# Performance work log

Measured on AMD Instinct MI355X. Metric: run time of the kernel, lower is better.

Reference implementation:

```python
import math
import jax, jax.numpy as jnp
import numpy as np

B, NP = 256, 3
LAT, TXT, D = 512, 768, 768
NL = 6
DI, DS, DC = 2 * D, 16, 4
DTR = math.ceil(D / 16)
EPS = 1e-5


def _silu(x):
    return x * jax.nn.sigmoid(x)


def _layernorm(x, g, b):
    m = x.mean(-1, keepdims=True)
    v = ((x - m) ** 2).mean(-1, keepdims=True)
    return (x - m) / jnp.sqrt(v + EPS) * g + b


def _mamba(x, in_w, conv_w, conv_b, xproj_w, dt_w, dt_b, Alog, Dp, out_w):
    # x: [B, L, D]; standard Mamba(d_state=16, d_conv=4, expand=2)
    Bb, L, _ = x.shape
    xz = jnp.einsum('bld,ed->ble', x, in_w)          # [B, L, 2*DI]
    u, z = jnp.split(xz, 2, axis=-1)
    # depthwise causal conv (kernel DC, left pad DC-1, truncated to L)
    up = jnp.pad(u, ((0, 0), (DC - 1, 0), (0, 0)))
    uc = conv_b + sum(conv_w[:, k] * up[:, k:k + L, :] for k in range(DC))
    uc = _silu(uc)
    xdbl = jnp.einsum('bld,ed->ble', uc, xproj_w)    # [B, L, DTR+2*DS]
    dt, Bm, Cm = jnp.split(xdbl, [DTR, DTR + DS], axis=-1)
    dt = jax.nn.softplus(jnp.einsum('blr,dr->bld', dt, dt_w) + dt_b)  # [B,L,DI]
    A = -jnp.exp(Alog)                               # [DI, DS]

    def step(h, xs):
        dt_t, B_t, C_t, u_t = xs                     # [B,DI],[B,DS],[B,DS],[B,DI]
        dA = jnp.exp(dt_t[..., None] * A)            # [B,DI,DS]
        h = h * dA + (dt_t * u_t)[..., None] * B_t[:, None, :]
        y = jnp.einsum('bds,bs->bd', h, C_t)
        return h, y

    h0 = jnp.zeros((Bb, DI, DS), x.dtype)
    xs = (dt.transpose(1, 0, 2), Bm.transpose(1, 0, 2),
          Cm.transpose(1, 0, 2), uc.transpose(1, 0, 2))
    _, ys = jax.lax.scan(step, h0, xs)
    y = ys.transpose(1, 0, 2) + Dp * uc
    y = y * _silu(z)
    return jnp.einsum('bld,ed->ble', y, out_w)       # [B, L, D]


def _forward(z_noisy, timestep, text_emb,
             zin_w, zin_b, tin_w, tin_b, time_w, time_b, part_emb,
             local_w, local_b, f_w, f_b, fuse_w, fuse_b, final_w, final_b,
             ln_g, ln_b, m_in_w, m_conv_w, m_conv_b, m_xproj_w, m_dt_w,
             m_dt_b, m_Alog, m_Dp, m_out_w, oln_g, oln_b, zout_w, zout_b):
    z_feat = jnp.einsum('bpl,dl->bpd', z_noisy, zin_w) + zin_b + part_emb
    text_feat = (text_emb @ tin_w.T + tin_b)[:, None]            # [B,1,D]
    half = D // 2
    freqs = jnp.exp(-math.log(10000.0) * jnp.arange(half, dtype=jnp.float32) / half)
    targ = timestep.astype(jnp.float32)[:, None] * freqs
    temb = jnp.concatenate([jnp.cos(targ), jnp.sin(targ)], -1)   # [B,D]
    time_feat = (temb @ time_w.T + time_b)[:, None]              # [B,1,D]
    x = jnp.concatenate([time_feat, text_feat, z_feat], 1)       # [B,5,D]
    # sinusoidal position embedding (first 5 rows of max_len=10 table)
    pos = jnp.arange(5, dtype=jnp.float32)[:, None]
    div = jnp.exp(jnp.arange(0, D, 2, dtype=jnp.float32) * (-math.log(10000.0) / D))
    pe = jnp.zeros((5, D), jnp.float32)
    pe = pe.at[:, 0::2].set(jnp.sin(pos * div)).at[:, 1::2].set(jnp.cos(pos * div))
    x = x + pe[None]
    text_cond = x[:, 1, :]                                       # [B,D]
    for i in range(NL):
        residual = x
        xl = _silu(jnp.einsum('bld,ed->ble', x, local_w[i]) + local_b[i])
        y_rep = jnp.broadcast_to(text_cond[:, None, :], xl.shape)
        yhat = jnp.einsum('bld,ed->ble', jnp.concatenate([xl, y_rep], -1), f_w[i]) + f_b[i]
        y_gate = y_rep * jax.nn.sigmoid(yhat)
        xt = jnp.einsum('bld,ed->ble', jnp.concatenate([xl, y_gate], -1), fuse_w[i]) + fuse_b[i]
        mf = lambda v, d: _mamba(v, m_in_w[i, d], m_conv_w[i, d], m_conv_b[i, d],
                                 m_xproj_w[i, d], m_dt_w[i, d], m_dt_b[i, d],
                                 m_Alog[i, d], m_Dp[i, d], m_out_w[i, d])
        xf = mf(xt, 0)
        xb = jnp.flip(mf(jnp.flip(xt, 1), 1), 1)
        xo = jnp.einsum('bld,ed->ble', jnp.concatenate([xf, xb], -1), final_w[i]) + final_b[i]
        x = _layernorm(xo + residual, ln_g[i], ln_b[i])
    z_out = x[:, 2:, :]                                          # [B,3,D]
    return jnp.einsum('bpd,ld->bpl', _layernorm(z_out, oln_g, oln_b), zout_w) + zout_b


def setup_inputs() -> dict:
    key = jax.random.key(0)
    kit = iter(jax.random.split(key, 40))

    def rn(shape, s=0.02):
        return jax.random.normal(next(kit), shape, jnp.float32) * s

    inp = dict(
        z_noisy=jax.random.normal(next(kit), (B, NP, LAT), jnp.float32),
        text_emb=jax.random.normal(next(kit), (B, TXT), jnp.float32),
        zin_w=rn((D, LAT)), zin_b=jnp.zeros((D,), jnp.float32),
        tin_w=rn((D, TXT)), tin_b=jnp.zeros((D,), jnp.float32),
        time_w=rn((D, D)), time_b=jnp.zeros((D,), jnp.float32),
        part_emb=rn((1, NP, D)),
        local_w=rn((NL, D, D)), local_b=jnp.zeros((NL, D), jnp.float32),
        f_w=rn((NL, D, 2 * D)), f_b=jnp.zeros((NL, D), jnp.float32),
        fuse_w=rn((NL, D, 2 * D)), fuse_b=jnp.zeros((NL, D), jnp.float32),
        final_w=rn((NL, D, 2 * D)), final_b=jnp.zeros((NL, D), jnp.float32),
        ln_g=jnp.ones((NL, D), jnp.float32), ln_b=jnp.zeros((NL, D), jnp.float32),
        m_in_w=rn((NL, 2, 2 * DI, D)),
        m_conv_w=rn((NL, 2, DI, DC), 0.1),
        m_conv_b=jnp.zeros((NL, 2, DI), jnp.float32),
        m_xproj_w=rn((NL, 2, DTR + 2 * DS, DI)),
        m_dt_w=rn((NL, 2, DI, DTR), 0.1),
        m_dt_b=jnp.full((NL, 2, DI), -4.6, jnp.float32),
        m_Alog=jnp.tile(jnp.log(jnp.arange(1, DS + 1, dtype=jnp.float32)), (NL, 2, DI, 1)),
        m_Dp=jnp.ones((NL, 2, DI), jnp.float32),
        m_out_w=rn((NL, 2, D, DI)),
        oln_g=jnp.ones((D,), jnp.float32), oln_b=jnp.zeros((D,), jnp.float32),
        zout_w=rn((LAT, D)), zout_b=jnp.zeros((LAT,), jnp.float32),
        timestep=jax.random.randint(next(kit), (B,), 0, 1000),
    )
    return inp


def reference(z_noisy, text_emb, zin_w, zin_b, tin_w, tin_b, time_w, time_b,
              part_emb, local_w, local_b, f_w, f_b, fuse_w, fuse_b, final_w,
              final_b, ln_g, ln_b, m_in_w, m_conv_w, m_conv_b, m_xproj_w,
              m_dt_w, m_dt_b, m_Alog, m_Dp, m_out_w, oln_g, oln_b, zout_w,
              zout_b, timestep):
    return _forward(z_noisy, timestep, text_emb, zin_w, zin_b, tin_w, tin_b,
                    time_w, time_b, part_emb, local_w, local_b, f_w, f_b,
                    fuse_w, fuse_b, final_w, final_b, ln_g, ln_b, m_in_w,
                    m_conv_w, m_conv_b, m_xproj_w, m_dt_w, m_dt_b, m_Alog,
                    m_Dp, m_out_w, oln_g, oln_b, zout_w, zout_b)
```

## Files before the change

### kernel.cpp

```cpp
#include <hip/hip_runtime.h>
#include <hip/hip_bf16.h>
#include <math.h>

#define B_   256
#define NP_  3
#define LAT_ 512
#define TXT_ 768
#define D_   768
#define NL_  6
#define DI_  1536
#define DS_  16
#define DC_  4
#define DTR_ 48
#define L_   5
#define M_   (B_*L_)
#define EPS_ 1e-5f

#define OB_WBF    0ull
#define OB_XPP    139591680ull
#define OB_TEMB   144310272ull
#define OB_ZNORM  144703488ull
#define OB_XBF    145883136ull
#define OB_TCBF   147849216ull
#define OB_CAT1   148242432ull
#define OB_XTBF   152174592ull
#define OB_XZBF   154140672ull
#define OB_UCY    169869312ull
#define OB_CAT2   177733632ull
#define OB_X      181665792ull
#define OB_TC     185597952ull
#define OB_ZFEAT  187170816ull
#define OB_XO     189530112ull
#define OB_PART   193462272ull

#define WO_LOCAL  0u
#define WO_F      3538944u
#define WO_FUSE   10616832u
#define WO_FINAL  17694720u
#define WO_IN     24772608u
#define WO_OUT    53084160u
#define WO_ZIN    67239936u
#define WO_TIN    67633152u
#define WO_TIME   68222976u
#define WO_ZOUT   68812800u
#define WO_ZNOISY 69206016u
#define WO_TEXT   69599232u
#define WO_END    69795840u

#define CVT_BLOCKS  17040u
#define XPAD_BLOCKS 1152u
#define TEMB_BLOCKS 384u
#define PREP_BLOCKS (CVT_BLOCKS + XPAD_BLOCKS + TEMB_BLOCKS)

typedef __attribute__((ext_vector_type(4))) float floatx4;
typedef __attribute__((ext_vector_type(8))) short short8;
typedef __attribute__((ext_vector_type(8))) unsigned short ushort8v;
typedef __attribute__((ext_vector_type(4))) unsigned short ushort4v;

__device__ __forceinline__ float sigm(float v) { return 1.f / (1.f + expf(-v)); }
__device__ __forceinline__ float softplus(float v) {
    return fmaxf(v, 0.f) + log1pf(expf(-fabsf(v)));
}
__device__ __forceinline__ unsigned short bf16rn(float f) {
    unsigned int u = __builtin_bit_cast(unsigned int, f);
    u = (u + 0x7fffu + ((u >> 16) & 1u)) >> 16;
    return (unsigned short)u;
}
__device__ __forceinline__ float b2f(unsigned short u) {
    unsigned int x = ((unsigned int)u) << 16;
    return __builtin_bit_cast(float, x);
}

template<int N> __device__ __forceinline__ void waitv() {
    asm volatile("s_waitcnt vmcnt(%0)" :: "i"(N) : "memory");
}

struct CvtArgs { const float* s[12]; };

__global__ __launch_bounds__(256) void prep_kernel(
    CvtArgs a, unsigned short* __restrict__ dst,
    const float* __restrict__ xw, unsigned short* __restrict__ xpd,
    const int* __restrict__ ts, unsigned short* __restrict__ temb)
{
    unsigned bid = blockIdx.x;
    if (bid < CVT_BLOCKS) {
        constexpr unsigned ends[12] = {
            3538944u, 10616832u, 17694720u, 24772608u, 53084160u, 67239936u,
            67633152u, 68222976u, 68812800u, 69206016u, 69599232u, 69795840u };
        const unsigned wv = (bid * 256u + threadIdx.x) >> 6;
        const unsigned lane = threadIdx.x & 63u;
        const unsigned wbase = wv * 1024u;
        unsigned idxq[4];
        floatx4 v[4];
#pragma unroll
        for (int q = 0; q < 4; ++q) {
            unsigned gbase = wbase + (unsigned)q * 256u;
            int t = 0;
            while (gbase >= ends[t]) ++t;
            unsigned start = t ? ends[t - 1] : 0u;
            idxq[q] = gbase + lane * 4u;
            v[q] = __builtin_nontemporal_load((const floatx4*)(a.s[t] + (idxq[q] - start)));
        }
#pragma unroll
        for (int q = 0; q < 4; ++q) {
            ushort4v o = { bf16rn(v[q][0]), bf16rn(v[q][1]), bf16rn(v[q][2]), bf16rn(v[q][3]) };
            __builtin_nontemporal_store(o, (ushort4v*)(dst + idxq[q]));
        }
    } else if (bid < CVT_BLOCKS + XPAD_BLOCKS) {
        unsigned i8 = ((bid - CVT_BLOCKS) * 256u + threadIdx.x) * 8u;
        if (i8 >= 12u * 128u * 1536u) return;
        unsigned pi = i8 / (128u * 1536u);
        unsigned rem = i8 - pi * 128u * 1536u;
        unsigned row = rem / 1536u, col = rem - row * 1536u;
        ushort8v o = {0, 0, 0, 0, 0, 0, 0, 0};
        if (row < 80u) {
            const float* s = xw + ((size_t)pi * 80u + row) * 1536u + col;
            floatx4 v0 = __builtin_nontemporal_load((const floatx4*)s);
            floatx4 v1 = __builtin_nontemporal_load((const floatx4*)(s + 4));
            o = ushort8v{ bf16rn(v0[0]), bf16rn(v0[1]), bf16rn(v0[2]), bf16rn(v0[3]),
                          bf16rn(v1[0]), bf16rn(v1[1]), bf16rn(v1[2]), bf16rn(v1[3]) };
        }
        *(ushort8v*)(xpd + i8) = o;
    } else {
        int idx = (bid - CVT_BLOCKS - XPAD_BLOCKS) * 256 + threadIdx.x;
        if (idx >= B_ * 384) return;
        int j = idx % 384, b = idx / 384;
        float f = expf(-logf(10000.f) * (float)j / 384.f);
        float targ = (float)ts[b] * f;
        temb[(size_t)b * D_ + j]       = bf16rn(cosf(targ));
        temb[(size_t)b * D_ + 384 + j] = bf16rn(sinf(targ));
    }
}

template<int BM, int BN, int CD, int DEPTH, int PF>
__global__ __launch_bounds__(256) void gemm_bf16_kernel(
    const unsigned short* __restrict__ A, int lda,
    const unsigned short* __restrict__ W, int wld,
    const float* __restrict__ bias,
    const float* __restrict__ aux0,
    const float* __restrict__ aux1,
    void* __restrict__ Cv, int ldc,
    int M, int N, int K, int epi, int ncap,
    int zsplit, unsigned long long zA, unsigned long long zW, unsigned long long zC)
{
    constexpr int GA = BM / 64;
    constexpr int GB = BN / 64;
    constexpr int LPS = GA + GB;
    constexpr int FRM = BM / 32;
    constexpr int FRN = BN / 32;
    constexpr int BMSK = DEPTH - 1;

    const int z = blockIdx.z;
    const int dirz = z / zsplit, ksz = z - dirz * zsplit;
    A += (unsigned long long)dirz * zA + (unsigned long long)ksz * (unsigned)K;
    W += (unsigned long long)dirz * zW + (unsigned long long)ksz * (unsigned)K;

    __shared__ unsigned short lds[DEPTH][(BM + BN) * 32];

    const int tid = threadIdx.x;
    const int m0 = blockIdx.y * BM, n0 = blockIdx.x * BN;
    const int w = tid >> 6, lane = tid & 63;
    const int wr = w >> 1, wc = w & 1;
    const int lrow = lane & 15;
    const int lk = (lane >> 4) << 3;

    const int rA = tid >> 2, sA = tid & 3;
    const int scA = ((sA ^ ((rA >> 1) & 3)) << 3);
    floatx4 acc[FRM][FRN] = {};

    auto stage = [&](int buf, int k0) {
        unsigned short* base = &lds[buf][0];
#pragma unroll
        for (int i = 0; i < GA; ++i) {
            int t = tid + i * 256;
            int r = t >> 2;
            const unsigned short* src = A + (size_t)(m0 + r) * lda + k0 + scA;
            __builtin_amdgcn_global_load_lds(
                (const __attribute__((address_space(1))) unsigned int*)(const void*)src,
                (__attribute__((address_space(3))) unsigned int*)(void*)(base + i * 2048 + w * 512),
                16, 0, 0);
        }
#pragma unroll
        for (int i = 0; i < GB; ++i) {
            int t = tid + i * 256;
            int r = t >> 2;
            const unsigned short* src = W + (size_t)(n0 + r) * wld + k0 + scA;
            __builtin_amdgcn_global_load_lds(
                (const __attribute__((address_space(1))) unsigned int*)(const void*)src,
                (__attribute__((address_space(3))) unsigned int*)(void*)(base + BM * 32 + i * 2048 + w * 512),
                16, 0, 0);
        }
    };

    const int nt = K >> 5;
#pragma unroll
    for (int s = 0; s < PF; ++s)
        if (s < nt) stage(s, s << 5);

    int offA[FRM], offB[FRN];
#pragma unroll
    for (int i = 0; i < FRM; ++i) {
        int row = wr * (BM / 2) + i * 16 + lrow;
        offA[i] = row * 32 + (lk ^ (((row >> 1) & 3) << 3));
    }
#pragma unroll
    for (int j = 0; j < FRN; ++j) {
        int row = wc * (BN / 2) + j * 16 + lrow;
        offB[j] = BM * 32 + row * 32 + (lk ^ (((row >> 1) & 3) << 3));
    }

    for (int t = 0; t < nt; ++t) {
        int rem = nt - 1 - t;
        if (rem >= PF) { stage((t + PF) & BMSK, (t + PF) << 5); waitv<PF * LPS>(); }
        else if (rem == 5) waitv<5 * LPS>();
        else if (rem == 4) waitv<4 * LPS>();
        else if (rem == 3) waitv<3 * LPS>();
        else if (rem == 2) waitv<2 * LPS>();
        else if (rem == 1) waitv<1 * LPS>();
        else               waitv<0>();
        __builtin_amdgcn_s_barrier();
        const unsigned short* pl = &lds[t & BMSK][0];
        short8 af[FRM], bfv[FRN];
#pragma unroll
        for (int i = 0; i < FRM; ++i) af[i] = *(const short8*)(pl + offA[i]);
#pragma unroll
        for (int j = 0; j < FRN; ++j) bfv[j] = *(const short8*)(pl + offB[j]);
#pragma unroll
        for (int i = 0; i < FRM; ++i)
#pragma unroll
            for (int j = 0; j < FRN; ++j)
                acc[i][j] = __builtin_amdgcn_mfma_f32_16x16x32_bf16(af[i], bfv[j], acc[i][j], 0, 0, 0);
    }

#pragma unroll
    for (int i = 0; i < FRM; ++i) {
        int row0 = m0 + wr * (BM / 2) + i * 16 + (lane >> 4) * 4;
#pragma unroll
        for (int j = 0; j < FRN; ++j) {
            int col = n0 + wc * (BN / 2) + j * 16 + lrow;
            if (col >= ncap) continue;
            float bb = bias ? bias[col] : 0.f;
#pragma unroll
            for (int r = 0; r < 4; ++r) {
                int row = row0 + r;
                float v = acc[i][j][r] + bb;
                if (epi == 1) {
                    v = v * sigm(v);
                } else if (epi == 3) {
                    int b = row / 5;
                    v = acc[i][j][r] + bb + b2f(((const unsigned short*)aux0)[(size_t)b * 768 + col]);
                    v = aux1[(size_t)b * 768 + col] * sigm(v);
                }
                size_t off = (size_t)z * zC + (size_t)row * ldc + col;
                if (CD == 1) ((float*)Cv)[off] = v;
                else         ((unsigned short*)Cv)[off] = bf16rn(v);
            }
        }
    }
}

template<int CD, int DEPTH, int PF>
__global__ __launch_bounds__(512) void gemm512_kernel(
    const unsigned short* __restrict__ A, int lda,
    const unsigned short* __restrict__ W, int wld,
    const float* __restrict__ bias,
    const float* __restrict__ aux0,
    const float* __restrict__ aux1,
    void* __restrict__ Cv, int ldc,
    int M, int N, int K, int epi, int ncap,
    int zsplit, unsigned long long zA, unsigned long long zW, unsigned long long zC)
{
    constexpr int BMSK = DEPTH - 1;
    const int z = blockIdx.z;
    const int dirz = z / zsplit, ksz = z - dirz * zsplit;
    A += (unsigned long long)dirz * zA + (unsigned long long)ksz * (unsigned)K;
    W += (unsigned long long)dirz * zW + (unsigned long long)ksz * (unsigned)K;

    __shared__ unsigned short lds[DEPTH][128 * 32];

    const int tid = threadIdx.x;
    const int m0 = blockIdx.y * 64, n0 = blockIdx.x * 64;
    const int w = tid >> 6, lane = tid & 63;
    const int wr = w >> 1, wc = w & 1;
    const int lrow = lane & 15;
    const int lk = (lane >> 4) << 3;

    const int st = tid & 255;
    const int rA = st >> 2, sA = st & 3;
    const int scA = ((sA ^ ((rA >> 1) & 3)) << 3);
    const bool isA = (tid < 256);
    floatx4 acc[2] = {};

    auto stage = [&](int buf, int k0) {
        unsigned short* dstp = &lds[buf][0] + (isA ? w * 512 : 2048 + (w - 4) * 512);
        const unsigned short* src = isA
            ? A + (size_t)(m0 + rA) * lda + k0 + scA
            : W + (size_t)(n0 + rA) * wld + k0 + scA;
        __builtin_amdgcn_global_load_lds(
            (const __attribute__((address_space(1))) unsigned int*)(const void*)src,
            (__attribute__((address_space(3))) unsigned int*)(void*)dstp,
            16, 0, 0);
    };

    const int nt = K >> 5;
#pragma unroll
    for (int s = 0; s < PF; ++s)
        if (s < nt) stage(s, s << 5);

    const int rowA = wr * 16 + lrow;
    const int offA = rowA * 32 + (lk ^ (((rowA >> 1) & 3) << 3));
    int offB[2];
#pragma unroll
    for (int j = 0; j < 2; ++j) {
        int rowB = wc * 32 + j * 16 + lrow;
        offB[j] = 2048 + rowB * 32 + (lk ^ (((rowB >> 1) & 3) << 3));
    }

    for (int t = 0; t < nt; ++t) {
        int rem = nt - 1 - t;
        if (rem >= PF) { stage((t + PF) & BMSK, (t + PF) << 5); waitv<PF>(); }
        else if (rem == 5) waitv<5>();
        else if (rem == 4) waitv<4>();
        else if (rem == 3) waitv<3>();
        else if (rem == 2) waitv<2>();
        else if (rem == 1) waitv<1>();
        else               waitv<0>();
        __builtin_amdgcn_s_barrier();
        const unsigned short* pl = &lds[t & BMSK][0];
        short8 af = *(const short8*)(pl + offA);
        short8 b0 = *(const short8*)(pl + offB[0]);
        short8 b1 = *(const short8*)(pl + offB[1]);
        acc[0] = __builtin_amdgcn_mfma_f32_16x16x32_bf16(af, b0, acc[0], 0, 0, 0);
        acc[1] = __builtin_amdgcn_mfma_f32_16x16x32_bf16(af, b1, acc[1], 0, 0, 0);
    }

    int row0 = m0 + wr * 16 + (lane >> 4) * 4;
#pragma unroll
    for (int j = 0; j < 2; ++j) {
        int col = n0 + wc * 32 + j * 16 + lrow;
        if (col >= ncap) continue;
        float bb = bias ? bias[col] : 0.f;
#pragma unroll
        for (int r = 0; r < 4; ++r) {
            int row = row0 + r;
            float v = acc[j][r] + bb;
            if (epi == 1) {
                v = v * sigm(v);
            } else if (epi == 3) {
                int b = row / 5;
                v = acc[j][r] + bb + b2f(((const unsigned short*)aux0)[(size_t)b * 768 + col]);
                v = aux1[(size_t)b * 768 + col] * sigm(v);
            }
            size_t off = (size_t)z * zC + (size_t)row * ldc + col;
            if (CD == 1) ((float*)Cv)[off] = v;
            else         ((unsigned short*)Cv)[off] = bf16rn(v);
        }
    }
}

template<int DEPTH, int PF>
__global__ __launch_bounds__(512) void gemm512b_kernel(
    const unsigned short* __restrict__ A, int lda,
    const unsigned short* __restrict__ W, int wld,
    unsigned short* __restrict__ C, int ldc, int K)
{
    constexpr int BMSK = DEPTH - 1;
    __shared__ unsigned short lds[DEPTH][8192];

    const int tid = threadIdx.x;
    const int m0 = blockIdx.y * 128, n0 = blockIdx.x * 128;
    const int w = tid >> 6, lane = tid & 63;
    const int wr = w >> 2, wc = w & 3;
    const int lrow = lane & 15;
    const int lk = (lane >> 4) << 3;

    const int rA = tid >> 2, sA = tid & 3;
    const int scA = ((sA ^ ((rA >> 1) & 3)) << 3);
    floatx4 acc[4][2] = {};

    auto stage = [&](int buf, int k0) {
        unsigned short* base = &lds[buf][0];
        const unsigned short* srcA = A + (size_t)(m0 + rA) * lda + k0 + scA;
        __builtin_amdgcn_global_load_lds(
            (const __attribute__((address_space(1))) unsigned int*)(const void*)srcA,
            (__attribute__((address_space(3))) unsigned int*)(void*)(base + w * 512),
            16, 0, 0);
        const unsigned short* srcB = W + (size_t)(n0 + rA) * wld + k0 + scA;
        __builtin_amdgcn_global_load_lds(
            (const __attribute__((address_space(1))) unsigned int*)(const void*)srcB,
            (__attribute__((address_space(3))) unsigned int*)(void*)(base + 4096 + w * 512),
            16, 0, 0);
    };

    const int nt = K >> 5;
#pragma unroll
    for (int s = 0; s < PF; ++s)
        if (s < nt) stage(s, s << 5);

    int offA[4], offB[2];
#pragma unroll
    for (int i = 0; i < 4; ++i) {
        int row = wr * 64 + i * 16 + lrow;
        offA[i] = row * 32 + (lk ^ (((row >> 1) & 3) << 3));
    }
#pragma unroll
    for (int j = 0; j < 2; ++j) {
        int row = wc * 32 + j * 16 + lrow;
        offB[j] = 4096 + row * 32 + (lk ^ (((row >> 1) & 3) << 3));
    }

    for (int t = 0; t < nt; ++t) {
        int rem = nt - 1 - t;
        if (rem >= PF) { stage((t + PF) & BMSK, (t + PF) << 5); waitv<PF * 2>(); }
        else if (rem == 1) waitv<2>();
        else               waitv<0>();
        __builtin_amdgcn_s_barrier();
        const unsigned short* pl = &lds[t & BMSK][0];
        short8 af[4], bfv[2];
#pragma unroll
        for (int i = 0; i < 4; ++i) af[i] = *(const short8*)(pl + offA[i]);
#pragma unroll
        for (int j = 0; j < 2; ++j) bfv[j] = *(const short8*)(pl + offB[j]);
#pragma unroll
        for (int i = 0; i < 4; ++i)
#pragma unroll
            for (int j = 0; j < 2; ++j)
                acc[i][j] = __builtin_amdgcn_mfma_f32_16x16x32_bf16(af[i], bfv[j], acc[i][j], 0, 0, 0);
    }

#pragma unroll
    for (int i = 0; i < 4; ++i) {
        int row0 = m0 + wr * 64 + i * 16 + (lane >> 4) * 4;
#pragma unroll
        for (int j = 0; j < 2; ++j) {
            int col = n0 + wc * 32 + j * 16 + lrow;
#pragma unroll
            for (int r = 0; r < 4; ++r)
                C[(size_t)(row0 + r) * ldc + col] = bf16rn(acc[i][j][r]);
        }
    }
}

__global__ void finalize_embed_kernel(float* __restrict__ x,
                                      unsigned short* __restrict__ xbf,
                                      const float* __restrict__ zfeat,
                                      const float* __restrict__ part_emb,
                                      float* __restrict__ tc,
                                      unsigned short* __restrict__ tcbf)
{
    int idx = blockIdx.x * blockDim.x + threadIdx.x;
    if (idx >= B_ * L_ * D_) return;
    int d = idx % D_;
    int bl = idx / D_;
    int l = bl % L_, b = bl / L_;
    float v;
    if (l >= 2) v = zfeat[((size_t)(b * 3 + (l - 2))) * D_ + d] + part_emb[(size_t)(l - 2) * D_ + d];
    else        v = x[idx];
    int j = d >> 1;
    float dv = expf((float)(2 * j) * (-logf(10000.f) / (float)D_));
    float ang = (float)l * dv;
    v += (d & 1) ? cosf(ang) : sinf(ang);
    x[idx] = v;
    xbf[idx] = bf16rn(v);
    if (l == 1) { tc[(size_t)b * D_ + d] = v; tcbf[(size_t)b * D_ + d] = bf16rn(v); }
}

__global__ __launch_bounds__(256) void conv_silu_kernel(
    const unsigned short* __restrict__ xz,
    const float* __restrict__ cw,
    const float* __restrict__ cb,
    unsigned short* __restrict__ ucy)
{
    int idx = blockIdx.x * 256 + threadIdx.x;
    if (idx >= 2 * M_ * DI_ / 8) return;
    int c8 = (idx % (DI_ / 8)) * 8;
    int t2 = idx / (DI_ / 8);
    int bl = t2 % M_, dir = t2 / M_;
    int l = bl % L_, b = bl / L_;

    float acc[8];
    const float* cbp = cb + dir * DI_ + c8;
#pragma unroll
    for (int e = 0; e < 8; ++e) acc[e] = cbp[e];
    floatx4 w[8];
#pragma unroll
    for (int e = 0; e < 8; ++e)
        w[e] = *(const floatx4*)(cw + ((size_t)(dir * DI_ + c8 + e)) * DC_);
#pragma unroll
    for (int k = 0; k < DC_; ++k) {
        int lp = dir ? (l + 3 - k) : (l + k - 3);
        if (lp >= 0 && lp < L_) {
            ushort8v xv = *(const ushort8v*)(xz + ((size_t)(b * L_ + lp)) * 6144 + dir * 3072 + c8);
#pragma unroll
            for (int e = 0; e < 8; ++e) acc[e] = fmaf(w[e][k], b2f(xv[e]), acc[e]);
        }
    }
    ushort8v o;
#pragma unroll
    for (int e = 0; e < 8; ++e) { float v = acc[e]; o[e] = bf16rn(v * sigm(v)); }
    *(ushort8v*)(ucy + (size_t)idx * 8) = o;
}

__global__ __launch_bounds__(256) void dtscan_kernel(
    const float* __restrict__ part,
    unsigned short* ucy,
    const unsigned short* __restrict__ xz,
    const float* __restrict__ dt_w,
    const float* __restrict__ dt_b,
    const float* __restrict__ Alog,
    const float* __restrict__ Dp)
{
    __shared__ float xd[L_][80];
    const int dir = blockIdx.z;
    const int b = blockIdx.y;
    const int ch = blockIdx.x * 256 + threadIdx.x;

    for (int o = threadIdx.x; o < L_ * 80; o += 256) {
        int l = o / 80, n = o - l * 80;
        float s = 0.f;
#pragma unroll
        for (int ks = 0; ks < 8; ++ks)
            s += part[((size_t)(dir * 8 + ks) * M_ + b * L_ + l) * 80 + n];
        xd[l][n] = s;
    }
    __syncthreads();

    const int cg = dir * DI_ + ch;
    float dt[L_];
    const float* wp = dt_w + (size_t)cg * DTR_;
    float dbv = dt_b[cg];
#pragma unroll
    for (int l = 0; l < L_; ++l) {
        float v = dbv;
#pragma unroll
        for (int r = 0; r < DTR_; ++r) v = fmaf(xd[l][r], wp[r], v);
        dt[l] = softplus(v);
    }

    float Aa[DS_], h[DS_];
#pragma unroll
    for (int s = 0; s < DS_; ++s) { Aa[s] = -expf(Alog[(size_t)cg * DS_ + s]); h[s] = 0.f; }
    float Dv = Dp[cg];

#pragma unroll
    for (int t = 0; t < L_; ++t) {
        const int l = dir ? (L_ - 1 - t) : t;
        size_t base = (size_t)(b * L_ + l);
        size_t uoff = ((size_t)dir * M_ + base) * DI_ + ch;
        float dtv = dt[l];
        float ucv = b2f(ucy[uoff]);
        float du = dtv * ucv;
        float y = 0.f;
#pragma unroll
        for (int s = 0; s < DS_; ++s) {
            h[s] = h[s] * expf(dtv * Aa[s]) + du * xd[l][48 + s];
            y = fmaf(h[s], xd[l][64 + s], y);
        }
        float zv = b2f(xz[base * 6144 + dir * 3072 + 1536 + ch]);
        ucy[uoff] = bf16rn((y + Dv * ucv) * (zv * sigm(zv)));
    }
}

__device__ __forceinline__ float block_sum(float v)
{
    __shared__ float sd[4];
#pragma unroll
    for (int o = 1; o < 64; o <<= 1) v += __shfl_xor(v, o, 64);
    int lane = threadIdx.x & 63, wid = threadIdx.x >> 6;
    if (lane == 0) sd[wid] = v;
    __syncthreads();
    v = sd[0] + sd[1] + sd[2] + sd[3];
    __syncthreads();
    return v;
}

__global__ __launch_bounds__(256) void ln_residual_kernel(
    const float* __restrict__ xo, float* __restrict__ x,
    unsigned short* __restrict__ xbf,
    const float* __restrict__ g, const float* __restrict__ bt,
    const float* __restrict__ og, const float* __restrict__ ob,
    unsigned short* __restrict__ znorm, int do_out)
{
    int row = blockIdx.x;
    const float* pa = xo + (size_t)row * D_;
    float* px = x + (size_t)row * D_;
    float v[3];
    float s = 0.f;
#pragma unroll
    for (int i = 0; i < 3; ++i) { int d = threadIdx.x + 256 * i; v[i] = pa[d] + px[d]; s += v[i]; }
    float mean = block_sum(s) * (1.f / (float)D_);
    float sq = 0.f;
#pragma unroll
    for (int i = 0; i < 3; ++i) { float t = v[i] - mean; sq += t * t; }
    float var = block_sum(sq) * (1.f / (float)D_);
    float inv = rsqrtf(var + EPS_);
    float o[3];
#pragma unroll
    for (int i = 0; i < 3; ++i) {
        int d = threadIdx.x + 256 * i;
        o[i] = (v[i] - mean) * inv * g[d] + bt[d];
        px[d] = o[i];
        xbf[(size_t)row * D_ + d] = bf16rn(o[i]);
    }
    int l = row % L_;
    if (do_out && l >= 2) {
        int b = row / L_;
        float s2 = o[0] + o[1] + o[2];
        float mean2 = block_sum(s2) * (1.f / (float)D_);
        float sq2 = 0.f;
#pragma unroll
        for (int i = 0; i < 3; ++i) { float t = o[i] - mean2; sq2 += t * t; }
        float var2 = block_sum(sq2) * (1.f / (float)D_);
        float inv2 = rsqrtf(var2 + EPS_);
#pragma unroll
        for (int i = 0; i < 3; ++i) {
            int d = threadIdx.x + 256 * i;
            znorm[((size_t)(b * 3 + (l - 2))) * D_ + d] = bf16rn((o[i] - mean2) * inv2 * og[d] + ob[d]);
        }
    }
}

extern "C" void kernel_launch(void* const* d_in, const int* in_sizes, int n_in,
                              void* d_out, int out_size, void* d_ws, size_t ws_size,
                              hipStream_t stream)
{
    const float* z_noisy  = (const float*)d_in[0];
    const float* text_emb = (const float*)d_in[1];
    const float* zin_b    = (const float*)d_in[3];
    const float* tin_b    = (const float*)d_in[5];
    const float* time_b   = (const float*)d_in[7];
    const float* part_emb = (const float*)d_in[8];
    const float* local_b  = (const float*)d_in[10];
    const float* f_b      = (const float*)d_in[12];
    const float* fuse_b   = (const float*)d_in[14];
    const float* final_b  = (const float*)d_in[16];
    const float* ln_g     = (const float*)d_in[17];
    const float* ln_b     = (const float*)d_in[18];
    const float* m_conv_w = (const float*)d_in[20];
    const float* m_conv_b = (const float*)d_in[21];
    const float* m_xproj_w= (const float*)d_in[22];
    const float* m_dt_w   = (const float*)d_in[23];
    const float* m_dt_b   = (const float*)d_in[24];
    const float* m_Alog   = (const float*)d_in[25];
    const float* m_Dp     = (const float*)d_in[26];
    const float* oln_g    = (const float*)d_in[28];
    const float* oln_b    = (const float*)d_in[29];
    const float* zout_b   = (const float*)d_in[31];
    const int*   timestep = (const int*)d_in[32];

    char* wsb = (char*)d_ws;
    unsigned short* wbf   = (unsigned short*)(wsb + OB_WBF);
    unsigned short* xpp   = (unsigned short*)(wsb + OB_XPP);
    unsigned short* tembb = (unsigned short*)(wsb + OB_TEMB);
    unsigned short* znormb= (unsigned short*)(wsb + OB_ZNORM);
    unsigned short* xbf   = (unsigned short*)(wsb + OB_XBF);
    unsigned short* tcbf  = (unsigned short*)(wsb + OB_TCBF);
    unsigned short* cat1b = (unsigned short*)(wsb + OB_CAT1);
    unsigned short* xtbf  = (unsigned short*)(wsb + OB_XTBF);
    unsigned short* xzbf  = (unsigned short*)(wsb + OB_XZBF);
    unsigned short* ucy   = (unsigned short*)(wsb + OB_UCY);
    unsigned short* cat2b = (unsigned short*)(wsb + OB_CAT2);
    float* x     = (float*)(wsb + OB_X);
    float* tc    = (float*)(wsb + OB_TC);
    float* zfeat = (float*)(wsb + OB_ZFEAT);
    unsigned short* tcf6 = (unsigned short*)(wsb + OB_ZFEAT);
    float* xo    = (float*)(wsb + OB_XO);
    float* part  = (float*)(wsb + OB_PART);

    unsigned short* local_bf = wbf + WO_LOCAL;
    unsigned short* f_bf     = wbf + WO_F;
    unsigned short* fuse_bf  = wbf + WO_FUSE;
    unsigned short* final_bf = wbf + WO_FINAL;
    unsigned short* in_bf    = wbf + WO_IN;
    unsigned short* out_bf   = wbf + WO_OUT;
    unsigned short* zin_bf   = wbf + WO_ZIN;
    unsigned short* tin_bf   = wbf + WO_TIN;
    unsigned short* time_bf  = wbf + WO_TIME;
    unsigned short* zout_bf  = wbf + WO_ZOUT;
    unsigned short* znz_bf   = wbf + WO_ZNOISY;
    unsigned short* text_bf  = wbf + WO_TEXT;

    auto ew = [&](int n) { return dim3((n + 255) / 256); };

    CvtArgs ca;
    ca.s[0] = (const float*)d_in[9];
    ca.s[1] = (const float*)d_in[11];
    ca.s[2] = (const float*)d_in[13];
    ca.s[3] = (const float*)d_in[15];
    ca.s[4] = (const float*)d_in[19];
    ca.s[5] = (const float*)d_in[27];
    ca.s[6] = (const float*)d_in[2];
    ca.s[7] = (const float*)d_in[4];
    ca.s[8] = (const float*)d_in[6];
    ca.s[9] = (const float*)d_in[30];
    ca.s[10] = z_noisy;
    ca.s[11] = text_emb;
    hipLaunchKernelGGL(prep_kernel, dim3(PREP_BLOCKS), dim3(256), 0, stream,
                       ca, wbf, m_xproj_w, xpp, timestep, tembb);

    auto g512 = [&](const unsigned short* A, int lda, const unsigned short* W, int wld,
                    const float* bias, const float* a0, const float* a1,
                    void* C, int ldc, int Mm, int Nn, int Kk, int epi, int ncap, int cd,
                    int gz, int zsplit, unsigned long long zA, unsigned long long zW,
                    unsigned long long zC) {
        dim3 g(Nn / 64, Mm / 64, gz);
        if (cd == 1)
            gemm512_kernel<1, 8, 6><<<g, dim3(512), 0, stream>>>(
                A, lda, W, wld, bias, a0, a1, C, ldc, Mm, Nn, Kk, epi, ncap, zsplit, zA, zW, zC);
        else
            gemm512_kernel<0, 8, 6><<<g, dim3(512), 0, stream>>>(
                A, lda, W, wld, bias, a0, a1, C, ldc, Mm, Nn, Kk, epi, ncap, zsplit, zA, zW, zC);
    };
    auto g64s = [&](const unsigned short* A, int lda, const unsigned short* W, int wld,
                    const float* bias, const float* a0, const float* a1,
                    void* C, int ldc, int Mm, int Nn, int Kk, int epi, int ncap, int cd,
                    int gz, int zsplit, unsigned long long zA, unsigned long long zW,
                    unsigned long long zC) {
        dim3 g(Nn / 64, Mm / 64, gz);
        if (cd == 1)
            gemm_bf16_kernel<64, 64, 1, 4, 2><<<g, dim3(256), 0, stream>>>(
                A, lda, W, wld, bias, a0, a1, C, ldc, Mm, Nn, Kk, epi, ncap, zsplit, zA, zW, zC);
        else
            gemm_bf16_kernel<64, 64, 0, 4, 2><<<g, dim3(256), 0, stream>>>(
                A, lda, W, wld, bias, a0, a1, C, ldc, Mm, Nn, Kk, epi, ncap, zsplit, zA, zW, zC);
    };

    g512(tembb, D_, time_bf, D_, time_b, nullptr, nullptr, x, L_ * D_, B_, D_, D_, 0, D_, 1,
         1, 1, 0, 0, 0);
    g512(text_bf, TXT_, tin_bf, TXT_, tin_b, nullptr, nullptr, x + D_, L_ * D_, B_, D_, TXT_, 0, D_, 1,
         1, 1, 0, 0, 0);
    g512(znz_bf, LAT_, zin_bf, LAT_, zin_b, nullptr, nullptr, zfeat, D_, B_ * NP_, D_, LAT_, 0, D_, 1,
         1, 1, 0, 0, 0);
    hipLaunchKernelGGL(finalize_embed_kernel, ew(B_ * L_ * D_), dim3(256), 0, stream,
                       x, xbf, zfeat, part_emb, tc, tcbf);

    g512(tcbf, D_, f_bf + D_, 2 * D_, nullptr, nullptr, nullptr,
         tcf6, D_, B_, D_, D_, 0, D_, 0,
         6, 1, 0ull, (unsigned long long)D_ * 2 * D_, (unsigned long long)B_ * D_);

    for (int i = 0; i < NL_; ++i) {
        g512(xbf, D_, local_bf + (size_t)i * D_ * D_, D_, local_b + (size_t)i * D_,
             nullptr, nullptr, cat1b, 2 * D_, M_, D_, D_, 1, D_, 0, 1, 1, 0, 0, 0);
        g512(cat1b, 2 * D_, f_bf + (size_t)i * D_ * 2 * D_, 2 * D_, f_b + (size_t)i * D_,
             (const float*)(tcf6 + (size_t)i * B_ * D_), tc,
             cat1b + D_, 2 * D_, M_, D_, D_, 3, D_, 0, 1, 1, 0, 0, 0);
        g512(cat1b, 2 * D_, fuse_bf + (size_t)i * D_ * 2 * D_, 2 * D_, fuse_b + (size_t)i * D_,
             nullptr, nullptr, xtbf, D_, M_, D_, 2 * D_, 0, D_, 0, 1, 1, 0, 0, 0);

        {
            dim3 g(6144 / 128, M_ / 128, 1);
            gemm512b_kernel<4, 2><<<g, dim3(512), 0, stream>>>(
                xtbf, D_, in_bf + (size_t)i * 4718592ull, D_, xzbf, 6144, D_);
        }
        hipLaunchKernelGGL(conv_silu_kernel, dim3(2 * M_ * DI_ / 8 / 256), dim3(256), 0, stream,
                           xzbf, m_conv_w + (size_t)i * 2 * DI_ * DC_,
                           m_conv_b + (size_t)i * 2 * DI_, ucy);
        g64s(ucy, DI_, xpp + (size_t)i * 2 * 128 * DI_, DI_, nullptr, nullptr, nullptr,
             part, 80, M_, 128, 192, 0, 80, 1,
             16, 8, (unsigned long long)M_ * DI_, (unsigned long long)128 * DI_,
             (unsigned long long)M_ * 80);
        hipLaunchKernelGGL(dtscan_kernel, dim3(DI_ / 256, B_, 2), dim3(256), 0, stream,
                           part, ucy, xzbf,
                           m_dt_w + (size_t)i * 2 * DI_ * DTR_, m_dt_b + (size_t)i * 2 * DI_,
                           m_Alog + (size_t)i * 2 * DI_ * DS_, m_Dp + (size_t)i * 2 * DI_);
        g512(ucy, DI_, out_bf + (size_t)i * 2 * D_ * DI_, DI_, nullptr, nullptr, nullptr,
             cat2b, 2 * D_, M_, D_, DI_, 0, D_, 0,
             2, 1, (unsigned long long)M_ * DI_, (unsigned long long)D_ * DI_, 768ull);
        g512(cat2b, 2 * D_, final_bf + (size_t)i * D_ * 2 * D_, 2 * D_, final_b + (size_t)i * D_,
             nullptr, nullptr, xo, D_, M_, D_, 2 * D_, 0, D_, 1, 1, 1, 0, 0, 0);
        hipLaunchKernelGGL(ln_residual_kernel, dim3(M_), dim3(256), 0, stream,
                           xo, x, xbf, ln_g + (size_t)i * D_, ln_b + (size_t)i * D_,
                           oln_g, oln_b, znormb, (i == NL_ - 1) ? 1 : 0);
    }

    g512(znormb, D_, zout_bf, D_, zout_b, nullptr, nullptr,
         (float*)d_out, LAT_, B_ * NP_, LAT_, D_, 0, LAT_, 1, 1, 1, 0, 0, 0);
}
```

Before: 1.057 ms.

## Split K across wave groups in 64x64 GEMM with LDS reduction

Reorganizes the 512-thread 64x64 GEMM so each wave computes a 32x32 sub-tile (2x2 MFMAs) instead of 16x32, with the two groups of four waves taking alternating K-steps. A final LDS reduction adds the partial accumulators before the epilogue. This is meant to raise fragment reuse and cut LDS reads per MFMA. In exchange, half the waves sit idle each K-step, and the kernel adds an extra reduction pass with two barriers.

```diff
diff --git a/kernel.cpp b/kernel.cpp
--- a/kernel.cpp
+++ b/kernel.cpp
@@ -260,7 +260,7 @@
 }
 
 template<int CD, int DEPTH, int PF>
-__global__ __launch_bounds__(512) void gemm512_kernel(
+__global__ __launch_bounds__(512) void gemm512p_kernel(
     const unsigned short* __restrict__ A, int lda,
     const unsigned short* __restrict__ W, int wld,
     const float* __restrict__ bias,
@@ -281,7 +281,8 @@
     const int tid = threadIdx.x;
     const int m0 = blockIdx.y * 64, n0 = blockIdx.x * 64;
     const int w = tid >> 6, lane = tid & 63;
-    const int wr = w >> 1, wc = w & 1;
+    const int q = w & 3, p = w >> 2;
+    const int qr = q >> 1, qc = q & 1;
     const int lrow = lane & 15;
     const int lk = (lane >> 4) << 3;
 
@@ -289,7 +290,7 @@
     const int rA = st >> 2, sA = st & 3;
     const int scA = ((sA ^ ((rA >> 1) & 3)) << 3);
     const bool isA = (tid < 256);
-    floatx4 acc[2] = {};
+    floatx4 acc[2][2] = {};
 
     auto stage = [&](int buf, int k0) {
         unsigned short* dstp = &lds[buf][0] + (isA ? w * 512 : 2048 + (w - 4) * 512);
@@ -307,13 +308,16 @@
     for (int s = 0; s < PF; ++s)
         if (s < nt) stage(s, s << 5);
 
-    const int rowA = wr * 16 + lrow;
-    const int offA = rowA * 32 + (lk ^ (((rowA >> 1) & 3) << 3));
-    int offB[2];
+    int offA[2], offB[2];
+#pragma unroll
+    for (int i = 0; i < 2; ++i) {
+        int row = qr * 32 + i * 16 + lrow;
+        offA[i] = row * 32 + (lk ^ (((row >> 1) & 3) << 3));
+    }
 #pragma unroll
     for (int j = 0; j < 2; ++j) {
-        int rowB = wc * 32 + j * 16 + lrow;
-        offB[j] = 2048 + rowB * 32 + (lk ^ (((rowB >> 1) & 3) << 3));
+        int row = qc * 32 + j * 16 + lrow;
+        offB[j] = 2048 + row * 32 + (lk ^ (((row >> 1) & 3) << 3));
     }
 
     for (int t = 0; t < nt; ++t) {
@@ -326,34 +330,55 @@
         else if (rem == 1) waitv<1>();
         else               waitv<0>();
         __builtin_amdgcn_s_barrier();
-        const unsigned short* pl = &lds[t & BMSK][0];
-        short8 af = *(const short8*)(pl + offA);
-        short8 b0 = *(const short8*)(pl + offB[0]);
-        short8 b1 = *(const short8*)(pl + offB[1]);
-        acc[0] = __builtin_amdgcn_mfma_f32_16x16x32_bf16(af, b0, acc[0], 0, 0, 0);
-        acc[1] = __builtin_amdgcn_mfma_f32_16x16x32_bf16(af, b1, acc[1], 0, 0, 0);
-    }
-
-    int row0 = m0 + wr * 16 + (lane >> 4) * 4;
-#pragma unroll
-    for (int j = 0; j < 2; ++j) {
-        int col = n0 + wc * 32 + j * 16 + lrow;
-        if (col >= ncap) continue;
-        float bb = bias ? bias[col] : 0.f;
-#pragma unroll
-        for (int r = 0; r < 4; ++r) {
-            int row = row0 + r;
-            float v = acc[j][r] + bb;
-            if (epi == 1) {
-                v = v * sigm(v);
-            } else if (epi == 3) {
-                int b = row / 5;
-                v = acc[j][r] + bb + b2f(((const unsigned short*)aux0)[(size_t)b * 768 + col]);
-                v = aux1[(size_t)b * 768 + col] * sigm(v);
+        if ((t & 1) == p) {
+            const unsigned short* pl = &lds[t & BMSK][0];
+            short8 a0 = *(const short8*)(pl + offA[0]);
+            short8 a1 = *(const short8*)(pl + offA[1]);
+            short8 b0 = *(const short8*)(pl + offB[0]);
+            short8 b1 = *(const short8*)(pl + offB[1]);
+            acc[0][0] = __builtin_amdgcn_mfma_f32_16x16x32_bf16(a0, b0, acc[0][0], 0, 0, 0);
+            acc[0][1] = __builtin_amdgcn_mfma_f32_16x16x32_bf16(a0, b1, acc[0][1], 0, 0, 0);
+            acc[1][0] = __builtin_amdgcn_mfma_f32_16x16x32_bf16(a1, b0, acc[1][0], 0, 0, 0);
+            acc[1][1] = __builtin_amdgcn_mfma_f32_16x16x32_bf16(a1, b1, acc[1][1], 0, 0, 0);
+        }
+    }
+
+    __syncthreads();
+    floatx4* red = (floatx4*)&lds[0][0];
+    if (p == 1) {
+#pragma unroll
+        for (int i = 0; i < 2; ++i)
+#pragma unroll
+            for (int j = 0; j < 2; ++j)
+                red[q * 256 + lane * 4 + i * 2 + j] = acc[i][j];
+    }
+    __syncthreads();
+    if (p == 0) {
+#pragma unroll
+        for (int i = 0; i < 2; ++i) {
+            int row0 = m0 + qr * 32 + i * 16 + (lane >> 4) * 4;
+#pragma unroll
+            for (int j = 0; j < 2; ++j) {
+                int col = n0 + qc * 32 + j * 16 + lrow;
+                if (col >= ncap) continue;
+                floatx4 sum = acc[i][j] + red[q * 256 + lane * 4 + i * 2 + j];
+                float bb = bias ? bias[col] : 0.f;
+#pragma unroll
+                for (int r = 0; r < 4; ++r) {
+                    int row = row0 + r;
+                    float v = sum[r] + bb;
+                    if (epi == 1) {
+                        v = v * sigm(v);
+                    } else if (epi == 3) {
+                        int b = row / 5;
+                        v = sum[r] + bb + b2f(((const unsigned short*)aux0)[(size_t)b * 768 + col]);
+                        v = aux1[(size_t)b * 768 + col] * sigm(v);
+                    }
+                    size_t off = (size_t)z * zC + (size_t)row * ldc + col;
+                    if (CD == 1) ((float*)Cv)[off] = v;
+                    else         ((unsigned short*)Cv)[off] = bf16rn(v);
+                }
             }
-            size_t off = (size_t)z * zC + (size_t)row * ldc + col;
-            if (CD == 1) ((float*)Cv)[off] = v;
-            else         ((unsigned short*)Cv)[off] = bf16rn(v);
         }
     }
 }
@@ -705,10 +730,10 @@
                     unsigned long long zC) {
         dim3 g(Nn / 64, Mm / 64, gz);
         if (cd == 1)
-            gemm512_kernel<1, 8, 6><<<g, dim3(512), 0, stream>>>(
+            gemm512p_kernel<1, 8, 6><<<g, dim3(512), 0, stream>>>(
                 A, lda, W, wld, bias, a0, a1, C, ldc, Mm, Nn, Kk, epi, ncap, zsplit, zA, zW, zC);
         else
-            gemm512_kernel<0, 8, 6><<<g, dim3(512), 0, stream>>>(
+            gemm512p_kernel<0, 8, 6><<<g, dim3(512), 0, stream>>>(
                 A, lda, W, wld, bias, a0, a1, C, ldc, Mm, Nn, Kk, epi, ncap, zsplit, zA, zW, zC);
     };
     auto g64s = [&](const unsigned short* A, int lda, const unsigned short* W, int wld,
```

New measurement: 1.126 ms. 1.07x slower.
